# Kernel optimization log

Measured on AMD Instinct MI355X. Metric: run time of the kernel, lower is better.

## Reference

```python
import jax, jax.numpy as jnp
import numpy as np
import math

B, LC, LQ, D = 64, 1024, 128, 128


def setup_inputs() -> dict:
    key = jax.random.key(0)
    k1, k2, k3, k4, k5 = jax.random.split(key, 5)
    c_rep = jax.random.normal(k1, (B, LC, D), dtype=jnp.float32)
    q_rep = jax.random.normal(k2, (B, LQ, D), dtype=jnp.float32)
    c_mask = jax.random.randint(k3, (B, LC), 0, 2, dtype=jnp.int32)
    q_mask = jax.random.randint(k4, (B, LQ), 0, 2, dtype=jnp.int32)
    lim = math.sqrt(1.0 / D)
    w = jax.random.uniform(k5, (3 * D,), dtype=jnp.float32, minval=-lim, maxval=lim)
    return {"c_rep": c_rep, "q_rep": q_rep, "c_mask": c_mask, "q_mask": q_mask, "w": w}


def _mask_logits(t, m):
    # mask == 1 means masked (matches original: target*(1-mask) + mask*-1e30)
    return t * (1.0 - m) + m * (-1e30)


def reference(c_rep, q_rep, c_mask, q_mask, w):
    d = c_rep.shape[-1]
    w1, w2, w3 = w[:d], w[d:2 * d], w[2 * d:]
    # Trilinear similarity S[b,i,j] = <ct,w1> + <qt,w2> + <ct*qt,w3>
    # computed without materializing the [B,Lc,Lq,3D] concat tensor.
    S = (c_rep @ w1)[:, :, None] \
        + (q_rep @ w2)[:, None, :] \
        + jnp.einsum('bid,bjd->bij', c_rep * w3, q_rep)  # [B, Lc, Lq]
    qm = q_mask[:, None, :].astype(S.dtype)  # [B, 1, Lq]
    cm = c_mask[:, :, None].astype(S.dtype)  # [B, Lc, 1]
    S1 = jax.nn.softmax(_mask_logits(S, qm), axis=2)  # softmax over query dim
    S2 = jax.nn.softmax(_mask_logits(S, cm), axis=1)  # softmax over context dim
    A = jnp.einsum('bij,bjd->bid', S1, q_rep)  # [B, Lc, D]
    # B_att = S1 @ S2^T @ c_rep, associated right-first to avoid [B,Lc,Lc]
    T = jnp.einsum('bkj,bkd->bjd', S2, c_rep)  # [B, Lq, D]
    B_att = jnp.einsum('bij,bjd->bid', S1, T)  # [B, Lc, D]
    out = jnp.concatenate([c_rep, A, c_rep * A, c_rep * B_att], axis=2)  # [B, Lc, 4D]
    # dropout is identity at inference
    return out
```

## Files before the change

kernel.cpp:

```cpp
#include <hip/hip_runtime.h>
#include <hip/hip_bf16.h>
#include <cstdint>
#include <cstddef>

#define B_   64
#define LC_  1024
#define LQ_  128
#define D_   128

typedef __bf16 bf16;
typedef bf16  bf16x8 __attribute__((ext_vector_type(8)));
typedef bf16  bf16x4 __attribute__((ext_vector_type(4)));
typedef float f32x4  __attribute__((ext_vector_type(4)));

__device__ __forceinline__ f32x4 mfma16(bf16x8 a, bf16x8 b, f32x4 c) {
  return __builtin_amdgcn_mfma_f32_16x16x32_bf16(a, b, c, 0, 0, 0);
}

__device__ __forceinline__ int swz(int row, int elem) { return elem ^ ((row & 7) << 3); }

__global__ __launch_bounds__(256) void k0c(const float* __restrict__ c, const float* __restrict__ w,
                                           float* __restrict__ cw1, bf16* __restrict__ cw3,
                                           bf16* __restrict__ cT) {
  __shared__ float w1s[128];
  __shared__ float w3s[128];
  __shared__ bf16  ctile[128 * 132];
  const int b = blockIdx.y, ks = blockIdx.x;
  const int k0 = ks * 128;
  const int t = threadIdx.x;
  if (t < 128) { w1s[t] = w[t]; w3s[t] = w[256 + t]; }
  __syncthreads();
  {
    const int r = t >> 1, d0 = (t & 1) * 64;
    const float* crow = c + ((size_t)(b * LC_ + k0 + r) * D_ + d0);
    bf16* orow = cw3 + ((size_t)(b * LC_ + k0 + r) * D_ + d0);
    float dot = 0.f;
#pragma unroll
    for (int v = 0; v < 8; ++v) {
      const float4 f0 = ((const float4*)crow)[v * 2 + 0];
      const float4 f1 = ((const float4*)crow)[v * 2 + 1];
      const int dd = d0 + v * 8;
      dot += f0.x * w1s[dd + 0] + f0.y * w1s[dd + 1] + f0.z * w1s[dd + 2] + f0.w * w1s[dd + 3]
           + f1.x * w1s[dd + 4] + f1.y * w1s[dd + 5] + f1.z * w1s[dd + 6] + f1.w * w1s[dd + 7];
      bf16* cr = &ctile[r * 132 + dd];
      cr[0] = (bf16)f0.x; cr[1] = (bf16)f0.y; cr[2] = (bf16)f0.z; cr[3] = (bf16)f0.w;
      cr[4] = (bf16)f1.x; cr[5] = (bf16)f1.y; cr[6] = (bf16)f1.z; cr[7] = (bf16)f1.w;
      bf16x8 o;
      o[0] = (bf16)(f0.x * w3s[dd + 0]); o[1] = (bf16)(f0.y * w3s[dd + 1]);
      o[2] = (bf16)(f0.z * w3s[dd + 2]); o[3] = (bf16)(f0.w * w3s[dd + 3]);
      o[4] = (bf16)(f1.x * w3s[dd + 4]); o[5] = (bf16)(f1.y * w3s[dd + 5]);
      o[6] = (bf16)(f1.z * w3s[dd + 6]); o[7] = (bf16)(f1.w * w3s[dd + 7]);
      *(bf16x8*)(orow + v * 8) = o;
    }
    dot += __shfl_xor(dot, 1);
    if ((t & 1) == 0) cw1[b * LC_ + k0 + r] = dot;
  }
  __syncthreads();
  {
    const int d = t >> 1, kh = (t & 1) * 64;
    bf16* trow = cT + ((size_t)(b * D_ + d) * LC_ + k0 + kh);
#pragma unroll
    for (int v = 0; v < 8; ++v) {
      bf16x8 o;
#pragma unroll
      for (int e = 0; e < 8; ++e) o[e] = ctile[(kh + v * 8 + e) * 132 + d];
      *(bf16x8*)(trow + v * 8) = o;
    }
  }
}

__global__ __launch_bounds__(256) void k0q(const float* __restrict__ q, const float* __restrict__ w,
                                           float* __restrict__ qw2, bf16* __restrict__ qb,
                                           bf16* __restrict__ qT) {
  __shared__ float w2s[128];
  __shared__ bf16  qtile[128 * 132];
  const int b = blockIdx.x;
  const int t = threadIdx.x;
  if (t < 128) w2s[t] = w[128 + t];
  __syncthreads();
  {
    const int r = t >> 1, d0 = (t & 1) * 64;
    const float* qrow = q + ((size_t)(b * LQ_ + r) * D_ + d0);
    bf16* orow = qb + ((size_t)(b * LQ_ + r) * D_ + d0);
    float dot = 0.f;
#pragma unroll
    for (int v = 0; v < 8; ++v) {
      const float4 f0 = ((const float4*)qrow)[v * 2 + 0];
      const float4 f1 = ((const float4*)qrow)[v * 2 + 1];
      const int dd = d0 + v * 8;
      dot += f0.x * w2s[dd + 0] + f0.y * w2s[dd + 1] + f0.z * w2s[dd + 2] + f0.w * w2s[dd + 3]
           + f1.x * w2s[dd + 4] + f1.y * w2s[dd + 5] + f1.z * w2s[dd + 6] + f1.w * w2s[dd + 7];
      bf16x8 o;
      o[0] = (bf16)f0.x; o[1] = (bf16)f0.y; o[2] = (bf16)f0.z; o[3] = (bf16)f0.w;
      o[4] = (bf16)f1.x; o[5] = (bf16)f1.y; o[6] = (bf16)f1.z; o[7] = (bf16)f1.w;
      bf16* qr = &qtile[r * 132 + dd];
#pragma unroll
      for (int e = 0; e < 8; ++e) qr[e] = o[e];
      *(bf16x8*)(orow + v * 8) = o;
    }
    dot += __shfl_xor(dot, 1);
    if ((t & 1) == 0) qw2[b * LQ_ + r] = dot;
  }
  __syncthreads();
  {
    const int d = t >> 1, jh = (t & 1) * 64;
    bf16* trow = qT + ((size_t)(b * D_ + d) * LQ_ + jh);
#pragma unroll
    for (int v = 0; v < 8; ++v) {
      bf16x8 o;
#pragma unroll
      for (int e = 0; e < 8; ++e) o[e] = qtile[(jh + v * 8 + e) * 132 + d];
      *(bf16x8*)(trow + v * 8) = o;
    }
  }
}

__global__ __launch_bounds__(256) void k1p(const float* __restrict__ cw1, const float* __restrict__ qw2,
                                           const int* __restrict__ cmask,
                                           const bf16* __restrict__ cw3, const bf16* __restrict__ cT,
                                           const bf16* __restrict__ qb,
                                           float* __restrict__ Tpart, float* __restrict__ lpart) {
  __shared__ bf16  qs[64 * 128];
  __shared__ bf16  PT[64 * 64];
  __shared__ float lred[4][64];
  const int bx = blockIdx.x;
  const int ks = bx >> 1, jh = bx & 1;
  const int b = blockIdx.y;
  const int j0g = jh * 64;
  const int t = threadIdx.x;
  const int wk = t >> 6, lane = t & 63, quad = lane >> 4, l15 = lane & 15;

#pragma unroll
  for (int idx = t; idx < 1024; idx += 256) {
    const int row = idx >> 4, ch = idx & 15;
    *(bf16x8*)&qs[row * 128 + swz(row, ch * 8)] =
        *(const bf16x8*)(qb + ((size_t)(b * LQ_ + j0g + row) * D_ + ch * 8));
  }
  const f32x4 z = {0.f, 0.f, 0.f, 0.f};
  f32x4 Tacc[4][2];
#pragma unroll
  for (int jt = 0; jt < 4; ++jt) { Tacc[jt][0] = z; Tacc[jt][1] = z; }
  float lacc[4] = {0.f, 0.f, 0.f, 0.f};
  float qv[4];
#pragma unroll
  for (int jt = 0; jt < 4; ++jt) qv[jt] = qw2[b * LQ_ + j0g + jt * 16 + l15];
  __syncthreads();

  for (int kt = 0; kt < 2; ++kt) {
    const int k0g = ks * 128 + kt * 64;

    f32x4 S[4] = {z, z, z, z};
#pragma unroll
    for (int kk = 0; kk < 4; ++kk) {
      const bf16x8 a = *(const bf16x8*)(cw3 +
          ((size_t)(b * LC_ + k0g + wk * 16 + l15) * D_ + kk * 32 + quad * 8));
#pragma unroll
      for (int jt = 0; jt < 4; ++jt) {
        const int jr = jt * 16 + l15;
        const bf16x8 bq = *(const bf16x8*)&qs[jr * 128 + swz(jr, kk * 32 + quad * 8)];
        S[jt] = mfma16(a, bq, S[jt]);
      }
    }
    float c1v[4]; int cmv[4];
#pragma unroll
    for (int rr = 0; rr < 4; ++rr) {
      const int krow = k0g + wk * 16 + quad * 4 + rr;
      c1v[rr] = cw1[b * LC_ + krow];
      cmv[rr] = cmask[b * LC_ + krow];
    }
#pragma unroll
    for (int jt = 0; jt < 4; ++jt) {
      bf16x4 pk;
#pragma unroll
      for (int rr = 0; rr < 4; ++rr) {
        const float p = cmv[rr] ? 0.f : __expf(S[jt][rr] + c1v[rr] + qv[jt]);
        lacc[jt] += p;
        pk[rr] = (bf16)p;
      }
      const int jr = jt * 16 + l15;
      *(bf16x4*)&PT[jr * 64 + swz(jr, wk * 16 + quad * 4)] = pk;
    }
    __syncthreads();

#pragma unroll
    for (int kk = 0; kk < 2; ++kk) {
      const bf16x8 bd0 = *(const bf16x8*)(cT +
          ((size_t)(b * D_ + wk * 32 + l15) * LC_ + k0g + kk * 32 + quad * 8));
      const bf16x8 bd1 = *(const bf16x8*)(cT +
          ((size_t)(b * D_ + wk * 32 + 16 + l15) * LC_ + k0g + kk * 32 + quad * 8));
#pragma unroll
      for (int jt = 0; jt < 4; ++jt) {
        const int jr = jt * 16 + l15;
        const bf16x8 aP = *(const bf16x8*)&PT[jr * 64 + swz(jr, kk * 32 + quad * 8)];
        Tacc[jt][0] = mfma16(aP, bd0, Tacc[jt][0]);
        Tacc[jt][1] = mfma16(aP, bd1, Tacc[jt][1]);
      }
    }
    __syncthreads();
  }

#pragma unroll
  for (int jt = 0; jt < 4; ++jt) {
    lacc[jt] += __shfl_xor(lacc[jt], 16);
    lacc[jt] += __shfl_xor(lacc[jt], 32);
  }
  if (lane < 16) {
#pragma unroll
    for (int jt = 0; jt < 4; ++jt) lred[wk][jt * 16 + l15] = lacc[jt];
  }
  __syncthreads();
  if (t < 64)
    lpart[(size_t)(b * 8 + ks) * 128 + j0g + t] =
        lred[0][t] + lred[1][t] + lred[2][t] + lred[3][t];

  float* tp = Tpart + ((size_t)(b * 8 + ks)) * (128 * 128);
#pragma unroll
  for (int jt = 0; jt < 4; ++jt)
#pragma unroll
    for (int dt = 0; dt < 2; ++dt)
#pragma unroll
      for (int rr = 0; rr < 4; ++rr)
        tp[(j0g + jt * 16 + quad * 4 + rr) * 128 + wk * 32 + dt * 16 + l15] =
            Tacc[jt][dt][rr];
}

__global__ __launch_bounds__(256) void k1r(const float* __restrict__ Tpart,
                                           const float* __restrict__ lpart,
                                           bf16* __restrict__ TT) {
  __shared__ float Tsum[32 * 132];
  __shared__ float linv[32];
  const int js = blockIdx.x, b = blockIdx.y;
  const int j0 = js * 32;
  const int t = threadIdx.x;
#pragma unroll
  for (int idx = t; idx < 1024; idx += 256) {
    const int row = idx >> 5, seg = idx & 31;
    float4 s = {0.f, 0.f, 0.f, 0.f};
#pragma unroll
    for (int i = 0; i < 8; ++i) {
      const float4 v = ((const float4*)(Tpart + ((size_t)(b * 8 + i)) * (128 * 128)) + j0 * 32)[idx];
      s.x += v.x; s.y += v.y; s.z += v.z; s.w += v.w;
    }
    *(float4*)&Tsum[row * 132 + seg * 4] = s;
  }
  if (t < 32) {
    float l = 0.f;
#pragma unroll
    for (int i = 0; i < 8; ++i) l += lpart[(size_t)(b * 8 + i) * 128 + j0 + t];
    linv[t] = 1.f / l;
  }
  __syncthreads();
  const int d = t >> 1, jhh = (t & 1) * 16;
  bf16x8 o0, o1;
#pragma unroll
  for (int e = 0; e < 8; ++e) {
    o0[e] = (bf16)(Tsum[(jhh + e) * 132 + d] * linv[jhh + e]);
    o1[e] = (bf16)(Tsum[(jhh + 8 + e) * 132 + d] * linv[jhh + 8 + e]);
  }
  bf16* dst = TT + ((size_t)(b * D_ + d) * LQ_ + j0 + jhh);
  *(bf16x8*)dst = o0;
  *(bf16x8*)(dst + 8) = o1;
}

__global__ __launch_bounds__(256, 4) void k2(const float* __restrict__ c, const float* __restrict__ cw1,
                                             const float* __restrict__ qw2, const int* __restrict__ qmask,
                                             const bf16* __restrict__ cw3, const bf16* __restrict__ qb,
                                             const bf16* __restrict__ qT, const bf16* __restrict__ TT,
                                             float* __restrict__ out) {
  __shared__ __align__(16) char smem[37888];
  bf16* qTs = (bf16*)(smem);
  bf16* TTs = (bf16*)(smem + 16384);
  bf16* P1  = (bf16*)(smem + 32768);
  float* A32 = (float*)(smem);
  float* B32 = (float*)(smem + 16896);
  const int it = blockIdx.x, b = blockIdx.y;
  const int i0 = it * 64;
  const int t = threadIdx.x;
  const int w = t >> 6, lane = t & 63, quad = lane >> 4, l15 = lane & 15;

  bf16x8 aF[4];
#pragma unroll
  for (int kk = 0; kk < 4; ++kk)
    aF[kk] = *(const bf16x8*)(cw3 +
        ((size_t)(b * LC_ + i0 + w * 16 + l15) * D_ + kk * 32 + quad * 8));
  float c1v[4];
#pragma unroll
  for (int rr = 0; rr < 4; ++rr)
    c1v[rr] = cw1[b * LC_ + i0 + w * 16 + quad * 4 + rr];

  const f32x4 z = {0.f, 0.f, 0.f, 0.f};
  f32x4 Aacc[8], Bacc[8];
#pragma unroll
  for (int n = 0; n < 8; ++n) { Aacc[n] = z; Bacc[n] = z; }
  float lacc[4] = {0.f, 0.f, 0.f, 0.f};

#pragma unroll
  for (int jh = 0; jh < 2; ++jh) {
#pragma unroll
    for (int idx = t; idx < 1024; idx += 256) {
      const int row = idx >> 3, ch = idx & 7;
      const int sc = (ch * 8) ^ ((row & 7) << 3);
      *(bf16x8*)&qTs[row * 64 + sc] =
          *(const bf16x8*)(qT + ((size_t)(b * D_ + row) * LQ_ + jh * 64 + ch * 8));
      *(bf16x8*)&TTs[row * 64 + sc] =
          *(const bf16x8*)(TT + ((size_t)(b * D_ + row) * LQ_ + jh * 64 + ch * 8));
    }
    __syncthreads();

#pragma unroll
    for (int jtl = 0; jtl < 2; ++jtl) {
      const int j0 = jh * 64 + jtl * 32;
      const float qv0 = qw2[b * LQ_ + j0 + l15];
      const float qv1 = qw2[b * LQ_ + j0 + 16 + l15];
      const int   qm0 = qmask[b * LQ_ + j0 + l15];
      const int   qm1 = qmask[b * LQ_ + j0 + 16 + l15];

      f32x4 S0 = z, S1 = z;
#pragma unroll
      for (int kk = 0; kk < 4; ++kk) {
        const bf16x8 b0 = *(const bf16x8*)(qb +
            ((size_t)(b * LQ_ + j0 + l15) * D_ + kk * 32 + quad * 8));
        const bf16x8 b1 = *(const bf16x8*)(qb +
            ((size_t)(b * LQ_ + j0 + 16 + l15) * D_ + kk * 32 + quad * 8));
        S0 = mfma16(aF[kk], b0, S0);
        S1 = mfma16(aF[kk], b1, S1);
      }
#pragma unroll
      for (int rr = 0; rr < 4; ++rr) {
        const float p0 = qm0 ? 0.f : __expf(S0[rr] + c1v[rr] + qv0);
        const float p1 = qm1 ? 0.f : __expf(S1[rr] + c1v[rr] + qv1);
        lacc[rr] += p0 + p1;
        P1[(w * 16 + quad * 4 + rr) * 40 + l15] = (bf16)p0;
        P1[(w * 16 + quad * 4 + rr) * 40 + 16 + l15] = (bf16)p1;
      }
      __syncthreads();

      const bf16x8 aP = *(bf16x8*)&P1[(w * 16 + l15) * 40 + quad * 8];
      const int cbase = jtl * 32 + quad * 8;
#pragma unroll
      for (int nt = 0; nt < 8; ++nt) {
        const int row = nt * 16 + l15;
        const int sc = cbase ^ ((row & 7) << 3);
        const bf16x8 bq = *(bf16x8*)&qTs[row * 64 + sc];
        const bf16x8 bt = *(bf16x8*)&TTs[row * 64 + sc];
        Aacc[nt] = mfma16(aP, bq, Aacc[nt]);
        Bacc[nt] = mfma16(aP, bt, Bacc[nt]);
      }
      __syncthreads();
    }
  }

#pragma unroll
  for (int rr = 0; rr < 4; ++rr) {
    float v = lacc[rr];
    v += __shfl_xor(v, 1); v += __shfl_xor(v, 2);
    v += __shfl_xor(v, 4); v += __shfl_xor(v, 8);
    lacc[rr] = 1.f / v;
  }

#pragma unroll
  for (int h = 0; h < 2; ++h) {
    if ((w >> 1) == h) {
      const int lrow0 = (w & 1) * 16 + quad * 4;
#pragma unroll
      for (int nt = 0; nt < 8; ++nt)
#pragma unroll
        for (int rr = 0; rr < 4; ++rr) {
          A32[(lrow0 + rr) * 132 + nt * 16 + l15] = Aacc[nt][rr] * lacc[rr];
          B32[(lrow0 + rr) * 132 + nt * 16 + l15] = Bacc[nt][rr] * lacc[rr];
        }
    }
    __syncthreads();
#pragma unroll
    for (int idx = t; idx < 1024; idx += 256) {
      const int lrow = idx >> 5, seg = idx & 31;
      const size_t grow = (size_t)(b * LC_ + i0 + h * 32 + lrow);
      const float4 c4 = ((const float4*)(c + grow * D_))[seg];
      const float4 a4 = *(float4*)&A32[lrow * 132 + seg * 4];
      const float4 b4 = *(float4*)&B32[lrow * 132 + seg * 4];
      float4* ob = (float4*)(out + grow * 512);
      ob[seg] = c4;
      ob[32 + seg] = a4;
      float4 ca; ca.x = c4.x * a4.x; ca.y = c4.y * a4.y; ca.z = c4.z * a4.z; ca.w = c4.w * a4.w;
      ob[64 + seg] = ca;
      float4 cb; cb.x = c4.x * b4.x; cb.y = c4.y * b4.y; cb.z = c4.z * b4.z; cb.w = c4.w * b4.w;
      ob[96 + seg] = cb;
    }
    __syncthreads();
  }
}

extern "C" void kernel_launch(void* const* d_in, const int* in_sizes, int n_in,
                              void* d_out, int out_size, void* d_ws, size_t ws_size,
                              hipStream_t stream) {
  (void)in_sizes; (void)n_in; (void)out_size; (void)ws_size;
  const float* c     = (const float*)d_in[0];
  const float* q     = (const float*)d_in[1];
  const int*   cmask = (const int*)d_in[2];
  const int*   qmask = (const int*)d_in[3];
  const float* w     = (const float*)d_in[4];
  float* out = (float*)d_out;

  char* ws = (char*)d_ws;
  float* cw1 = (float*)(ws + 0);
  float* qw2 = (float*)(ws + 262144);
  bf16*  cw3 = (bf16*)(ws + 294912);
  bf16*  cT  = (bf16*)(ws + 17072128);
  bf16*  qb  = (bf16*)(ws + 33849344);
  bf16*  qT  = (bf16*)(ws + 35946496);
  bf16*  TT  = (bf16*)(ws + 38043648);

  float* Tpart = out;
  float* lpart = out + 8388608;

  k0c<<<dim3(8, 64), 256, 0, stream>>>(c, w, cw1, cw3, cT);
  k0q<<<dim3(64), 256, 0, stream>>>(q, w, qw2, qb, qT);
  k1p<<<dim3(16, 64), 256, 0, stream>>>(cw1, qw2, cmask, cw3, cT, qb, Tpart, lpart);
  k1r<<<dim3(4, 64), 256, 0, stream>>>(Tpart, lpart, TT);
  k2<<<dim3(16, 64), 256, 0, stream>>>(c, cw1, qw2, qmask, cw3, qb, qT, TT, out);
}
```

Measured before the change: 238.8 us.

## Merge preprocessing kernels and fold partial-T reduction into last-arriving block

Combines the context and query preprocessing kernels into one launch, with the query work on an extra grid column. Replaces the separate Tpart reduction kernel with a per-batch atomic counter, so the last of the 16 blocks for a batch does the reduction and writes TT. This cuts launches from five to three and drops the inter-kernel gaps. The cost is that one block per batch runs the whole reduction serially, and the code now relies on threadfence/atomic ordering with a counter stored in scratch space inside the output buffer.

```diff
diff --git a/kernel.cpp b/kernel.cpp
--- a/kernel.cpp
+++ b/kernel.cpp
@@ -19,110 +19,113 @@
 
 __device__ __forceinline__ int swz(int row, int elem) { return elem ^ ((row & 7) << 3); }
 
-__global__ __launch_bounds__(256) void k0c(const float* __restrict__ c, const float* __restrict__ w,
-                                           float* __restrict__ cw1, bf16* __restrict__ cw3,
-                                           bf16* __restrict__ cT) {
-  __shared__ float w1s[128];
-  __shared__ float w3s[128];
-  __shared__ bf16  ctile[128 * 132];
-  const int b = blockIdx.y, ks = blockIdx.x;
-  const int k0 = ks * 128;
+__global__ __launch_bounds__(256) void kpre(const float* __restrict__ c, const float* __restrict__ q,
+                                            const float* __restrict__ w,
+                                            float* __restrict__ cw1, bf16* __restrict__ cw3,
+                                            bf16* __restrict__ cT,
+                                            float* __restrict__ qw2, bf16* __restrict__ qb,
+                                            bf16* __restrict__ qT, int* __restrict__ cnt) {
+  __shared__ float wA[128];
+  __shared__ float wB[128];
+  __shared__ bf16  tile[128 * 136];
+  const int b = blockIdx.y, bx = blockIdx.x;
   const int t = threadIdx.x;
-  if (t < 128) { w1s[t] = w[t]; w3s[t] = w[256 + t]; }
-  __syncthreads();
-  {
-    const int r = t >> 1, d0 = (t & 1) * 64;
-    const float* crow = c + ((size_t)(b * LC_ + k0 + r) * D_ + d0);
-    bf16* orow = cw3 + ((size_t)(b * LC_ + k0 + r) * D_ + d0);
-    float dot = 0.f;
-#pragma unroll
-    for (int v = 0; v < 8; ++v) {
-      const float4 f0 = ((const float4*)crow)[v * 2 + 0];
-      const float4 f1 = ((const float4*)crow)[v * 2 + 1];
-      const int dd = d0 + v * 8;
-      dot += f0.x * w1s[dd + 0] + f0.y * w1s[dd + 1] + f0.z * w1s[dd + 2] + f0.w * w1s[dd + 3]
-           + f1.x * w1s[dd + 4] + f1.y * w1s[dd + 5] + f1.z * w1s[dd + 6] + f1.w * w1s[dd + 7];
-      bf16* cr = &ctile[r * 132 + dd];
-      cr[0] = (bf16)f0.x; cr[1] = (bf16)f0.y; cr[2] = (bf16)f0.z; cr[3] = (bf16)f0.w;
-      cr[4] = (bf16)f1.x; cr[5] = (bf16)f1.y; cr[6] = (bf16)f1.z; cr[7] = (bf16)f1.w;
-      bf16x8 o;
-      o[0] = (bf16)(f0.x * w3s[dd + 0]); o[1] = (bf16)(f0.y * w3s[dd + 1]);
-      o[2] = (bf16)(f0.z * w3s[dd + 2]); o[3] = (bf16)(f0.w * w3s[dd + 3]);
-      o[4] = (bf16)(f1.x * w3s[dd + 4]); o[5] = (bf16)(f1.y * w3s[dd + 5]);
-      o[6] = (bf16)(f1.z * w3s[dd + 6]); o[7] = (bf16)(f1.w * w3s[dd + 7]);
-      *(bf16x8*)(orow + v * 8) = o;
-    }
-    dot += __shfl_xor(dot, 1);
-    if ((t & 1) == 0) cw1[b * LC_ + k0 + r] = dot;
-  }
-  __syncthreads();
-  {
-    const int d = t >> 1, kh = (t & 1) * 64;
-    bf16* trow = cT + ((size_t)(b * D_ + d) * LC_ + k0 + kh);
-#pragma unroll
-    for (int v = 0; v < 8; ++v) {
-      bf16x8 o;
-#pragma unroll
-      for (int e = 0; e < 8; ++e) o[e] = ctile[(kh + v * 8 + e) * 132 + d];
-      *(bf16x8*)(trow + v * 8) = o;
+
+  if (bx < 8) {
+    const int k0 = bx * 128;
+    if (t < 128) { wA[t] = w[t]; wB[t] = w[256 + t]; }
+    __syncthreads();
+    {
+      const int r = t >> 1, d0 = (t & 1) * 64;
+      const float* crow = c + ((size_t)(b * LC_ + k0 + r) * D_ + d0);
+      bf16* orow = cw3 + ((size_t)(b * LC_ + k0 + r) * D_ + d0);
+      float dot = 0.f;
+#pragma unroll
+      for (int v = 0; v < 8; ++v) {
+        const float4 f0 = ((const float4*)crow)[v * 2 + 0];
+        const float4 f1 = ((const float4*)crow)[v * 2 + 1];
+        const int dd = d0 + v * 8;
+        dot += f0.x * wA[dd + 0] + f0.y * wA[dd + 1] + f0.z * wA[dd + 2] + f0.w * wA[dd + 3]
+             + f1.x * wA[dd + 4] + f1.y * wA[dd + 5] + f1.z * wA[dd + 6] + f1.w * wA[dd + 7];
+        bf16x8 oc, o;
+        oc[0] = (bf16)f0.x; oc[1] = (bf16)f0.y; oc[2] = (bf16)f0.z; oc[3] = (bf16)f0.w;
+        oc[4] = (bf16)f1.x; oc[5] = (bf16)f1.y; oc[6] = (bf16)f1.z; oc[7] = (bf16)f1.w;
+        o[0] = (bf16)(f0.x * wB[dd + 0]); o[1] = (bf16)(f0.y * wB[dd + 1]);
+        o[2] = (bf16)(f0.z * wB[dd + 2]); o[3] = (bf16)(f0.w * wB[dd + 3]);
+        o[4] = (bf16)(f1.x * wB[dd + 4]); o[5] = (bf16)(f1.y * wB[dd + 5]);
+        o[6] = (bf16)(f1.z * wB[dd + 6]); o[7] = (bf16)(f1.w * wB[dd + 7]);
+        *(bf16x8*)&tile[r * 136 + dd] = oc;
+        *(bf16x8*)(orow + v * 8) = o;
+      }
+      dot += __shfl_xor(dot, 1);
+      if ((t & 1) == 0) cw1[b * LC_ + k0 + r] = dot;
+    }
+    __syncthreads();
+    {
+      const int d = t >> 1, kh = (t & 1) * 64;
+      bf16* trow = cT + ((size_t)(b * D_ + d) * LC_ + k0 + kh);
+#pragma unroll
+      for (int v = 0; v < 8; ++v) {
+        bf16x8 o;
+#pragma unroll
+        for (int e = 0; e < 8; ++e) o[e] = tile[(kh + v * 8 + e) * 136 + d];
+        *(bf16x8*)(trow + v * 8) = o;
+      }
+    }
+  } else {
+    if (t < 128) wA[t] = w[128 + t];
+    if (t == 0) cnt[b] = 0;
+    __syncthreads();
+    {
+      const int r = t >> 1, d0 = (t & 1) * 64;
+      const float* qrow = q + ((size_t)(b * LQ_ + r) * D_ + d0);
+      bf16* orow = qb + ((size_t)(b * LQ_ + r) * D_ + d0);
+      float dot = 0.f;
+#pragma unroll
+      for (int v = 0; v < 8; ++v) {
+        const float4 f0 = ((const float4*)qrow)[v * 2 + 0];
+        const float4 f1 = ((const float4*)qrow)[v * 2 + 1];
+        const int dd = d0 + v * 8;
+        dot += f0.x * wA[dd + 0] + f0.y * wA[dd + 1] + f0.z * wA[dd + 2] + f0.w * wA[dd + 3]
+             + f1.x * wA[dd + 4] + f1.y * wA[dd + 5] + f1.z * wA[dd + 6] + f1.w * wA[dd + 7];
+        bf16x8 o;
+        o[0] = (bf16)f0.x; o[1] = (bf16)f0.y; o[2] = (bf16)f0.z; o[3] = (bf16)f0.w;
+        o[4] = (bf16)f1.x; o[5] = (bf16)f1.y; o[6] = (bf16)f1.z; o[7] = (bf16)f1.w;
+        *(bf16x8*)&tile[r * 136 + dd] = o;
+        *(bf16x8*)(orow + v * 8) = o;
+      }
+      dot += __shfl_xor(dot, 1);
+      if ((t & 1) == 0) qw2[b * LQ_ + r] = dot;
+    }
+    __syncthreads();
+    {
+      const int d = t >> 1, jh = (t & 1) * 64;
+      bf16* trow = qT + ((size_t)(b * D_ + d) * LQ_ + jh);
+#pragma unroll
+      for (int v = 0; v < 8; ++v) {
+        bf16x8 o;
+#pragma unroll
+        for (int e = 0; e < 8; ++e) o[e] = tile[(jh + v * 8 + e) * 136 + d];
+        *(bf16x8*)(trow + v * 8) = o;
+      }
     }
   }
 }
 
-__global__ __launch_bounds__(256) void k0q(const float* __restrict__ q, const float* __restrict__ w,
-                                           float* __restrict__ qw2, bf16* __restrict__ qb,
-                                           bf16* __restrict__ qT) {
-  __shared__ float w2s[128];
-  __shared__ bf16  qtile[128 * 132];
-  const int b = blockIdx.x;
-  const int t = threadIdx.x;
-  if (t < 128) w2s[t] = w[128 + t];
-  __syncthreads();
-  {
-    const int r = t >> 1, d0 = (t & 1) * 64;
-    const float* qrow = q + ((size_t)(b * LQ_ + r) * D_ + d0);
-    bf16* orow = qb + ((size_t)(b * LQ_ + r) * D_ + d0);
-    float dot = 0.f;
-#pragma unroll
-    for (int v = 0; v < 8; ++v) {
-      const float4 f0 = ((const float4*)qrow)[v * 2 + 0];
-      const float4 f1 = ((const float4*)qrow)[v * 2 + 1];
-      const int dd = d0 + v * 8;
-      dot += f0.x * w2s[dd + 0] + f0.y * w2s[dd + 1] + f0.z * w2s[dd + 2] + f0.w * w2s[dd + 3]
-           + f1.x * w2s[dd + 4] + f1.y * w2s[dd + 5] + f1.z * w2s[dd + 6] + f1.w * w2s[dd + 7];
-      bf16x8 o;
-      o[0] = (bf16)f0.x; o[1] = (bf16)f0.y; o[2] = (bf16)f0.z; o[3] = (bf16)f0.w;
-      o[4] = (bf16)f1.x; o[5] = (bf16)f1.y; o[6] = (bf16)f1.z; o[7] = (bf16)f1.w;
-      bf16* qr = &qtile[r * 132 + dd];
-#pragma unroll
-      for (int e = 0; e < 8; ++e) qr[e] = o[e];
-      *(bf16x8*)(orow + v * 8) = o;
-    }
-    dot += __shfl_xor(dot, 1);
-    if ((t & 1) == 0) qw2[b * LQ_ + r] = dot;
-  }
-  __syncthreads();
-  {
-    const int d = t >> 1, jh = (t & 1) * 64;
-    bf16* trow = qT + ((size_t)(b * D_ + d) * LQ_ + jh);
-#pragma unroll
-    for (int v = 0; v < 8; ++v) {
-      bf16x8 o;
-#pragma unroll
-      for (int e = 0; e < 8; ++e) o[e] = qtile[(jh + v * 8 + e) * 132 + d];
-      *(bf16x8*)(trow + v * 8) = o;
-    }
-  }
-}
-
-__global__ __launch_bounds__(256) void k1p(const float* __restrict__ cw1, const float* __restrict__ qw2,
-                                           const int* __restrict__ cmask,
-                                           const bf16* __restrict__ cw3, const bf16* __restrict__ cT,
-                                           const bf16* __restrict__ qb,
-                                           float* __restrict__ Tpart, float* __restrict__ lpart) {
-  __shared__ bf16  qs[64 * 128];
-  __shared__ bf16  PT[64 * 64];
-  __shared__ float lred[4][64];
+__global__ __launch_bounds__(256) void k1(const float* __restrict__ cw1, const float* __restrict__ qw2,
+                                          const int* __restrict__ cmask,
+                                          const bf16* __restrict__ cw3, const bf16* __restrict__ cT,
+                                          const bf16* __restrict__ qb,
+                                          float* __restrict__ Tpart, float* __restrict__ lpart,
+                                          int* __restrict__ cnt, bf16* __restrict__ TT) {
+  __shared__ __align__(16) char smem[25600];
+  bf16* qs = (bf16*)smem;
+  bf16* PT = (bf16*)(smem + 16384);
+  float* lred = (float*)(smem + 24576);
+  float* Tsum = (float*)smem;
+  float* linv = (float*)(smem + 16896);
+  __shared__ int lastFlag;
+
   const int bx = blockIdx.x;
   const int ks = bx >> 1, jh = bx & 1;
   const int b = blockIdx.y;
@@ -206,12 +209,12 @@
   }
   if (lane < 16) {
 #pragma unroll
-    for (int jt = 0; jt < 4; ++jt) lred[wk][jt * 16 + l15] = lacc[jt];
+    for (int jt = 0; jt < 4; ++jt) lred[wk * 64 + jt * 16 + l15] = lacc[jt];
   }
   __syncthreads();
   if (t < 64)
     lpart[(size_t)(b * 8 + ks) * 128 + j0g + t] =
-        lred[0][t] + lred[1][t] + lred[2][t] + lred[3][t];
+        lred[0 * 64 + t] + lred[1 * 64 + t] + lred[2 * 64 + t] + lred[3 * 64 + t];
 
   float* tp = Tpart + ((size_t)(b * 8 + ks)) * (128 * 128);
 #pragma unroll
@@ -222,44 +225,46 @@
       for (int rr = 0; rr < 4; ++rr)
         tp[(j0g + jt * 16 + quad * 4 + rr) * 128 + wk * 32 + dt * 16 + l15] =
             Tacc[jt][dt][rr];
-}
-
-__global__ __launch_bounds__(256) void k1r(const float* __restrict__ Tpart,
-                                           const float* __restrict__ lpart,
-                                           bf16* __restrict__ TT) {
-  __shared__ float Tsum[32 * 132];
-  __shared__ float linv[32];
-  const int js = blockIdx.x, b = blockIdx.y;
-  const int j0 = js * 32;
-  const int t = threadIdx.x;
-#pragma unroll
-  for (int idx = t; idx < 1024; idx += 256) {
-    const int row = idx >> 5, seg = idx & 31;
-    float4 s = {0.f, 0.f, 0.f, 0.f};
-#pragma unroll
-    for (int i = 0; i < 8; ++i) {
-      const float4 v = ((const float4*)(Tpart + ((size_t)(b * 8 + i)) * (128 * 128)) + j0 * 32)[idx];
-      s.x += v.x; s.y += v.y; s.z += v.z; s.w += v.w;
-    }
-    *(float4*)&Tsum[row * 132 + seg * 4] = s;
-  }
-  if (t < 32) {
-    float l = 0.f;
-#pragma unroll
-    for (int i = 0; i < 8; ++i) l += lpart[(size_t)(b * 8 + i) * 128 + j0 + t];
-    linv[t] = 1.f / l;
-  }
+
+  __threadfence();
   __syncthreads();
-  const int d = t >> 1, jhh = (t & 1) * 16;
-  bf16x8 o0, o1;
-#pragma unroll
-  for (int e = 0; e < 8; ++e) {
-    o0[e] = (bf16)(Tsum[(jhh + e) * 132 + d] * linv[jhh + e]);
-    o1[e] = (bf16)(Tsum[(jhh + 8 + e) * 132 + d] * linv[jhh + 8 + e]);
-  }
-  bf16* dst = TT + ((size_t)(b * D_ + d) * LQ_ + j0 + jhh);
-  *(bf16x8*)dst = o0;
-  *(bf16x8*)(dst + 8) = o1;
+  if (t == 0) lastFlag = (atomicAdd(&cnt[b], 1) == 15);
+  __syncthreads();
+  if (!lastFlag) return;
+  __threadfence();
+
+  for (int js = 0; js < 4; ++js) {
+    const int j0 = js * 32;
+    __syncthreads();
+#pragma unroll
+    for (int idx = t; idx < 1024; idx += 256) {
+      const int row = idx >> 5, seg = idx & 31;
+      float4 s = {0.f, 0.f, 0.f, 0.f};
+#pragma unroll
+      for (int i = 0; i < 8; ++i) {
+        const float4 v = ((const float4*)(Tpart + ((size_t)(b * 8 + i)) * (128 * 128)) + j0 * 32)[idx];
+        s.x += v.x; s.y += v.y; s.z += v.z; s.w += v.w;
+      }
+      *(float4*)&Tsum[row * 132 + seg * 4] = s;
+    }
+    if (t < 32) {
+      float l = 0.f;
+#pragma unroll
+      for (int i = 0; i < 8; ++i) l += lpart[(size_t)(b * 8 + i) * 128 + j0 + t];
+      linv[t] = 1.f / l;
+    }
+    __syncthreads();
+    const int d = t >> 1, jhh = (t & 1) * 16;
+    bf16x8 o0, o1;
+#pragma unroll
+    for (int e = 0; e < 8; ++e) {
+      o0[e] = (bf16)(Tsum[(jhh + e) * 132 + d] * linv[jhh + e]);
+      o1[e] = (bf16)(Tsum[(jhh + 8 + e) * 132 + d] * linv[jhh + 8 + e]);
+    }
+    bf16* dst = TT + ((size_t)(b * D_ + d) * LQ_ + j0 + jhh);
+    *(bf16x8*)dst = o0;
+    *(bf16x8*)(dst + 8) = o1;
+  }
 }
 
 __global__ __launch_bounds__(256, 4) void k2(const float* __restrict__ c, const float* __restrict__ cw1,
@@ -412,10 +417,9 @@
 
   float* Tpart = out;
   float* lpart = out + 8388608;
-
-  k0c<<<dim3(8, 64), 256, 0, stream>>>(c, w, cw1, cw3, cT);
-  k0q<<<dim3(64), 256, 0, stream>>>(q, w, qw2, qb, qT);
-  k1p<<<dim3(16, 64), 256, 0, stream>>>(cw1, qw2, cmask, cw3, cT, qb, Tpart, lpart);
-  k1r<<<dim3(4, 64), 256, 0, stream>>>(Tpart, lpart, TT);
-  k2<<<dim3(16, 64), 256, 0, stream>>>(c, cw1, qw2, qmask, cw3, qb, qT, TT, out);
+  int*   cnt   = (int*)(out + 8454144);
+
+  kpre<<<dim3(9, 64), 256, 0, stream>>>(c, q, w, cw1, cw3, cT, qw2, qb, qT, cnt);
+  k1  <<<dim3(16, 64), 256, 0, stream>>>(cw1, qw2, cmask, cw3, cT, qb, Tpart, lpart, cnt, TT);
+  k2  <<<dim3(16, 64), 256, 0, stream>>>(c, cw1, qw2, qmask, cw3, qb, qT, TT, out);
 }
```

Measured after the change: 405.7 us. 1.7x slower.
